# Kernel optimization log

Hardware: AMD Instinct MI355X
Metric: run time of the kernel (lower is better)

## Reference

```python
import jax, jax.numpy as jnp
import numpy as np

B, N, D = 4, 512, 128
H1, H2 = 64, 32
NEG_SLOPE = 0.1

def _leaky(x):
    return jnp.where(x >= 0, x, NEG_SLOPE * x)

def setup_inputs() -> dict:
    key = jax.random.key(0)
    ks = jax.random.split(key, 7)
    v = jax.random.normal(ks[0], (B, N, D), dtype=jnp.float32)
    # 1x1 Conv2d weights collapse to [out, in] matrices
    W1 = jax.random.normal(ks[1], (H1, D), dtype=jnp.float32) * (1.0 / np.sqrt(D))
    b1 = jax.random.normal(ks[2], (H1,), dtype=jnp.float32) * 0.01
    W2 = jax.random.normal(ks[3], (H2, H1), dtype=jnp.float32) * (1.0 / np.sqrt(H1))
    b2 = jax.random.normal(ks[4], (H2,), dtype=jnp.float32) * 0.01
    W3 = jax.random.normal(ks[5], (1, H2), dtype=jnp.float32) * (1.0 / np.sqrt(H2))
    b3 = jax.random.normal(ks[6], (1,), dtype=jnp.float32) * 0.01
    return {"v": v, "W1": W1, "b1": b1, "W2": W2, "b2": b2, "W3": W3, "b3": b3}

def reference(v, W1, b1, W2, b2, W3, b3):
    # phi_ij = |v_i - v_j|  -> (B, N, N, D)
    phi = jnp.abs(v[:, :, None, :] - v[:, None, :, :])
    # 1x1 convs == per-(i,j) linear layers over the channel dim
    h = _leaky(jnp.einsum('bijd,od->bijo', phi, W1) + b1)   # (B,N,N,64)
    h = _leaky(jnp.einsum('bijc,oc->bijo', h, W2) + b2)     # (B,N,N,32)
    a = jnp.einsum('bijc,oc->bijo', h, W3) + b3             # (B,N,N,1)
    a = a[..., 0]                                           # (B,N,N)
    return jax.nn.softmax(a, axis=2)                        # softmax over neighbors j
```

## Files before the change

### kernel.cpp

```cpp
#include <hip/hip_runtime.h>

#define NN  512
#define DD  128
#define NTASK_B 8448
#define NWAVES  2048

typedef __attribute__((ext_vector_type(4))) float f32x4;
typedef __attribute__((ext_vector_type(8))) short s16x8;

#define MFMA(a, b, c) __builtin_amdgcn_mfma_f32_16x16x32_bf16((a), (b), (c), 0, 0, 0)

#define B1S 136
#define B2S 72
#define H1S 68

__device__ inline void split8(const float* __restrict__ x, s16x8& h, s16x8& l) {
    uint4 hp, lp;
    unsigned* hw = (unsigned*)&hp;
    unsigned* lw = (unsigned*)&lp;
    #pragma unroll
    for (int i = 0; i < 4; ++i) {
        float x0 = x[2 * i], x1 = x[2 * i + 1];
        unsigned t0 = __float_as_uint(x0) + 0x8000u;
        unsigned t1 = __float_as_uint(x1) + 0x8000u;
        hw[i] = __builtin_amdgcn_perm(t1, t0, 0x07060302u);
        float l0 = x0 - __uint_as_float(t0 & 0xFFFF0000u);
        float l1 = x1 - __uint_as_float(t1 & 0xFFFF0000u);
        lw[i] = __builtin_amdgcn_perm(__float_as_uint(l1), __float_as_uint(l0), 0x07060302u);
    }
    h = __builtin_bit_cast(s16x8, hp);
    l = __builtin_bit_cast(s16x8, lp);
}

__device__ inline void split1(float x, unsigned short& hs, unsigned short& ls) {
    unsigned t = __float_as_uint(x) + 0x8000u;
    hs = (unsigned short)(t >> 16);
    float lo = x - __uint_as_float(t & 0xFFFF0000u);
    ls = (unsigned short)(__float_as_uint(lo) >> 16);
}

__global__ __launch_bounds__(256, 2)
void adj_sym(const float* __restrict__ v,
             const float* __restrict__ W1,
             const float* __restrict__ b1,
             const float* __restrict__ W2,
             const float* __restrict__ b2,
             const float* __restrict__ W3,
             const float* __restrict__ b3,
             float* __restrict__ out)
{
    __shared__ __attribute__((aligned(16))) unsigned short B1h_s[64 * B1S];
    __shared__ __attribute__((aligned(16))) unsigned short B1l_s[64 * B1S];
    __shared__ __attribute__((aligned(16))) unsigned short B2h_s[32 * B2S];
    __shared__ __attribute__((aligned(16))) unsigned short B2l_s[32 * B2S];
    __shared__ __attribute__((aligned(16))) float h1_s[64 * H1S];

    const int t    = threadIdx.x;
    const int w    = t >> 6;
    const int lane = t & 63;
    const int m16  = t & 15;
    const int q    = (t & 63) >> 4;
    const int q8   = q * 8;

    #pragma unroll
    for (int e = 0; e < 32; ++e) {
        int idx = e * 256 + t;
        unsigned short hs, ls;
        split1(W1[idx], hs, ls);
        int o = idx >> 7, d = idx & 127;
        B1h_s[o * B1S + d] = hs;
        B1l_s[o * B1S + d] = ls;
    }
    #pragma unroll
    for (int e = 0; e < 8; ++e) {
        int idx = e * 256 + t;
        unsigned short hs, ls;
        split1(W2[idx], hs, ls);
        int c2 = idx >> 6, k = idx & 63;
        B2h_s[c2 * B2S + k] = hs;
        B2l_s[c2 * B2S + k] = ls;
    }

    float b1v[4];
    #pragma unroll
    for (int ot = 0; ot < 4; ++ot) b1v[ot] = b1[ot * 16 + m16];
    const float b2v0 = b2[m16];
    const float b2v1 = b2[16 + m16];
    const float w3v0 = W3[m16];
    const float w3v1 = W3[16 + m16];
    const float b3v  = b3[0];

    __syncthreads();

    const int g    = blockIdx.x * 4 + w;
    int       tk   = (33 * g) >> 1;
    const int tend = (33 * (g + 1)) >> 1;

    unsigned bb = (unsigned)tk / (unsigned)NTASK_B;
    int r = tk - (int)(bb * NTASK_B);
    int G = (int)((__fsqrt_rn((float)(2 * r + 1)) - 1.0f) * 0.25f);
    if (G < 0) G = 0;
    while (8 * (G + 1) * (G + 2) <= r) ++G;
    while (G > 0 && 8 * G * (G + 1) > r) --G;
    int rem = r - 8 * G * (G + 1);
    int s   = rem / (G + 1);
    int gj  = rem - s * (G + 1);
    bool newi = true;

    float yv[4][8];

    #pragma unroll 1
    for (; tk < tend; ++tk) {
        const int    i  = (G << 4) + s;
        const int    j0 = gj << 4;
        const size_t vb = ((size_t)bb << 9);

        if (newi) {
            const float* __restrict__ vip = v + (vb + i) * DD;
            #pragma unroll
            for (int kt = 0; kt < 4; ++kt) {
                *(float4*)&yv[kt][0] = *(const float4*)(vip + kt * 32 + q8);
                *(float4*)&yv[kt][4] = *(const float4*)(vip + kt * 32 + q8 + 4);
            }
        }

        const float* __restrict__ vr = v + (vb + j0 + m16) * DD;
        float xr[4][8];
        #pragma unroll
        for (int kt = 0; kt < 4; ++kt) {
            *(float4*)&xr[kt][0] = *(const float4*)(vr + kt * 32 + q8);
            *(float4*)&xr[kt][4] = *(const float4*)(vr + kt * 32 + q8 + 4);
        }

        f32x4 c[4];
        #pragma unroll
        for (int ot = 0; ot < 4; ++ot) c[ot] = (f32x4){0.f, 0.f, 0.f, 0.f};

        #pragma unroll
        for (int kt = 0; kt < 4; ++kt) {
            float d8[8];
            #pragma unroll
            for (int ii = 0; ii < 8; ++ii) d8[ii] = fabsf(yv[kt][ii] - xr[kt][ii]);
            s16x8 ah, al;
            split8(d8, ah, al);
            #pragma unroll
            for (int ot = 0; ot < 4; ++ot) {
                const int n = ot * 16 + m16;
                s16x8 bh = *(const s16x8*)(B1h_s + n * B1S + kt * 32 + q8);
                s16x8 bl = *(const s16x8*)(B1l_s + n * B1S + kt * 32 + q8);
                c[ot] = MFMA(ah, bh, c[ot]);
                c[ot] = MFMA(al, bh, c[ot]);
                c[ot] = MFMA(ah, bl, c[ot]);
            }
        }

        #pragma unroll
        for (int ot = 0; ot < 4; ++ot)
            #pragma unroll
            for (int rr = 0; rr < 4; ++rr) {
                float hv = c[ot][rr] + b1v[ot];
                hv = fmaxf(hv, 0.1f * hv);
                h1_s[(w * 16 + q * 4 + rr) * H1S + ot * 16 + m16] = hv;
            }

        f32x4 dacc[2];
        dacc[0] = (f32x4){0.f, 0.f, 0.f, 0.f};
        dacc[1] = (f32x4){0.f, 0.f, 0.f, 0.f};
        #pragma unroll
        for (int kt2 = 0; kt2 < 2; ++kt2) {
            const float* hp = h1_s + (w * 16 + m16) * H1S + kt2 * 32 + q8;
            float a8[8];
            *(float4*)&a8[0] = *(const float4*)(hp);
            *(float4*)&a8[4] = *(const float4*)(hp + 4);
            s16x8 ah, al;
            split8(a8, ah, al);
            #pragma unroll
            for (int ot2 = 0; ot2 < 2; ++ot2) {
                const int n = ot2 * 16 + m16;
                s16x8 bh = *(const s16x8*)(B2h_s + n * B2S + kt2 * 32 + q8);
                s16x8 bl = *(const s16x8*)(B2l_s + n * B2S + kt2 * 32 + q8);
                dacc[ot2] = MFMA(ah, bh, dacc[ot2]);
                dacc[ot2] = MFMA(al, bh, dacc[ot2]);
                dacc[ot2] = MFMA(ah, bl, dacc[ot2]);
            }
        }

        float sval[4];
        #pragma unroll
        for (int r2 = 0; r2 < 4; ++r2) {
            float h0  = dacc[0][r2] + b2v0;  h0  = fmaxf(h0, 0.1f * h0);
            float h1v = dacc[1][r2] + b2v1;  h1v = fmaxf(h1v, 0.1f * h1v);
            float sc = fmaf(w3v0, h0, w3v1 * h1v);
            sc += __shfl_xor(sc, 1, 64);
            sc += __shfl_xor(sc, 2, 64);
            sc += __shfl_xor(sc, 4, 64);
            sc += __shfl_xor(sc, 8, 64);
            sval[r2] = sc + b3v;
        }
        const int p = lane & 15;
        float vv = sval[0];
        vv = ((lane & 3) == 1) ? sval[1] : vv;
        vv = ((lane & 3) == 2) ? sval[2] : vv;
        vv = ((lane & 3) == 3) ? sval[3] : vv;
        const float pv = __shfl(vv, ((p >> 2) << 4) | (p & 3), 64);

        if (lane < 32) {
            const size_t addr = (lane < 16)
                ? (vb + (unsigned)i) * NN + (unsigned)(j0 + p)
                : (vb + (unsigned)(j0 + p)) * NN + (unsigned)i;
            out[addr] = pv;
        }

        ++gj;
        newi = false;
        if (gj > G) {
            gj = 0; newi = true;
            if (++s == 16) {
                s = 0;
                if (++G == 32) { G = 0; ++bb; }
            }
        }
    }
}

__global__ __launch_bounds__(256)
void row_softmax(float* __restrict__ out)
{
    __shared__ float red[8];
    const int t    = threadIdx.x;
    const int w    = t >> 6;
    const int lane = t & 63;

    float* orow = out + (size_t)blockIdx.x * NN;
    float a0 = orow[t];
    float a1 = orow[t + 256];

    float m = fmaxf(a0, a1);
    #pragma unroll
    for (int sh = 32; sh > 0; sh >>= 1)
        m = fmaxf(m, __shfl_xor(m, sh, 64));
    if (lane == 0) red[w] = m;
    __syncthreads();
    const float M = fmaxf(fmaxf(red[0], red[1]), fmaxf(red[2], red[3]));

    float e0 = __expf(a0 - M);
    float e1 = __expf(a1 - M);
    float s01 = e0 + e1;
    #pragma unroll
    for (int sh = 32; sh > 0; sh >>= 1)
        s01 += __shfl_xor(s01, sh, 64);
    if (lane == 0) red[4 + w] = s01;
    __syncthreads();
    const float S = (red[4] + red[5]) + (red[6] + red[7]);
    const float inv = 1.0f / S;

    orow[t]       = e0 * inv;
    orow[t + 256] = e1 * inv;
}

extern "C" void kernel_launch(void* const* d_in, const int* in_sizes, int n_in,
                              void* d_out, int out_size, void* d_ws, size_t ws_size,
                              hipStream_t stream) {
    const float* v  = (const float*)d_in[0];
    const float* W1 = (const float*)d_in[1];
    const float* b1 = (const float*)d_in[2];
    const float* W2 = (const float*)d_in[3];
    const float* b2 = (const float*)d_in[4];
    const float* W3 = (const float*)d_in[5];
    const float* b3 = (const float*)d_in[6];
    float* out = (float*)d_out;

    adj_sym<<<dim3(512), dim3(256), 0, stream>>>(v, W1, b1, W2, b2, W3, b3, out);
    row_softmax<<<dim3(4 * NN), dim3(256), 0, stream>>>(out);
}
```

Measured before the change: 118.0 us.

## Process two j-tiles per task and keep W2 split fragments in registers

Each wave task now covers 32 neighbour columns (two 16-wide j tiles) instead of 16. The two tiles share the B1 shared-memory fragment loads, and their MFMAs are interleaved to hide latency. W2 hi/lo bf16 fragments move from LDS into registers, h1 is stored in LDS pre-packed as hi/lo pairs, and the cross-lane reductions use DPP row rotates instead of shuffles. The task count and decode change to match. The costs are higher register pressure and wasted MFMA work on the odd diagonal tile, whose second half is computed but not stored.

```diff
diff --git a/kernel.cpp b/kernel.cpp
--- a/kernel.cpp
+++ b/kernel.cpp
@@ -2,8 +2,7 @@
 
 #define NN  512
 #define DD  128
-#define NTASK_B 8448
-#define NWAVES  2048
+#define NST_B 4352
 
 typedef __attribute__((ext_vector_type(4))) float f32x4;
 typedef __attribute__((ext_vector_type(8))) short s16x8;
@@ -11,8 +10,10 @@
 #define MFMA(a, b, c) __builtin_amdgcn_mfma_f32_16x16x32_bf16((a), (b), (c), 0, 0, 0)
 
 #define B1S 136
-#define B2S 72
 #define H1S 68
+
+#define ROR_ADD(x, CTRL) \
+    ((x) + __int_as_float(__builtin_amdgcn_update_dpp(0, __float_as_int(x), (CTRL), 0xF, 0xF, true)))
 
 __device__ inline void split8(const float* __restrict__ x, s16x8& h, s16x8& l) {
     uint4 hp, lp;
@@ -32,28 +33,38 @@
     l = __builtin_bit_cast(s16x8, lp);
 }
 
-__device__ inline void split1(float x, unsigned short& hs, unsigned short& ls) {
-    unsigned t = __float_as_uint(x) + 0x8000u;
-    hs = (unsigned short)(t >> 16);
-    float lo = x - __uint_as_float(t & 0xFFFF0000u);
-    ls = (unsigned short)(__float_as_uint(lo) >> 16);
+__device__ inline unsigned packhl(float x) {
+    unsigned tt = __float_as_uint(x) + 0x8000u;
+    float lo = x - __uint_as_float(tt & 0xFFFF0000u);
+    return __builtin_amdgcn_perm(__float_as_uint(lo), tt, 0x07060302u);
+}
+
+__device__ inline void unpack8(const unsigned* __restrict__ u, s16x8& h, s16x8& l) {
+    uint4 hp, lp;
+    unsigned* hw = (unsigned*)&hp;
+    unsigned* lw = (unsigned*)&lp;
+    #pragma unroll
+    for (int i = 0; i < 4; ++i) {
+        hw[i] = __builtin_amdgcn_perm(u[2 * i + 1], u[2 * i], 0x05040100u);
+        lw[i] = __builtin_amdgcn_perm(u[2 * i + 1], u[2 * i], 0x07060302u);
+    }
+    h = __builtin_bit_cast(s16x8, hp);
+    l = __builtin_bit_cast(s16x8, lp);
 }
 
 __global__ __launch_bounds__(256, 2)
-void adj_sym(const float* __restrict__ v,
-             const float* __restrict__ W1,
-             const float* __restrict__ b1,
-             const float* __restrict__ W2,
-             const float* __restrict__ b2,
-             const float* __restrict__ W3,
-             const float* __restrict__ b3,
-             float* __restrict__ out)
+void adj_sym2(const float* __restrict__ v,
+              const float* __restrict__ W1,
+              const float* __restrict__ b1,
+              const float* __restrict__ W2,
+              const float* __restrict__ b2,
+              const float* __restrict__ W3,
+              const float* __restrict__ b3,
+              float* __restrict__ out)
 {
     __shared__ __attribute__((aligned(16))) unsigned short B1h_s[64 * B1S];
     __shared__ __attribute__((aligned(16))) unsigned short B1l_s[64 * B1S];
-    __shared__ __attribute__((aligned(16))) unsigned short B2h_s[32 * B2S];
-    __shared__ __attribute__((aligned(16))) unsigned short B2l_s[32 * B2S];
-    __shared__ __attribute__((aligned(16))) float h1_s[64 * H1S];
+    __shared__ __attribute__((aligned(16))) unsigned h1p_s[64 * H1S];
 
     const int t    = threadIdx.x;
     const int w    = t >> 6;
@@ -63,23 +74,39 @@
     const int q8   = q * 8;
 
     #pragma unroll
-    for (int e = 0; e < 32; ++e) {
-        int idx = e * 256 + t;
-        unsigned short hs, ls;
-        split1(W1[idx], hs, ls);
-        int o = idx >> 7, d = idx & 127;
-        B1h_s[o * B1S + d] = hs;
-        B1l_s[o * B1S + d] = ls;
+    for (int e = 0; e < 8; ++e) {
+        int idx4 = e * 256 + t;
+        int o = idx4 >> 5;
+        int d = (idx4 & 31) * 4;
+        float4 x = *(const float4*)(W1 + idx4 * 4);
+        float xs[4] = {x.x, x.y, x.z, x.w};
+        unsigned tb[4], lb[4];
+        #pragma unroll
+        for (int k2 = 0; k2 < 4; ++k2) {
+            tb[k2] = __float_as_uint(xs[k2]) + 0x8000u;
+            float lo = xs[k2] - __uint_as_float(tb[k2] & 0xFFFF0000u);
+            lb[k2] = __float_as_uint(lo);
+        }
+        uint2 hw, lw;
+        hw.x = __builtin_amdgcn_perm(tb[1], tb[0], 0x07060302u);
+        hw.y = __builtin_amdgcn_perm(tb[3], tb[2], 0x07060302u);
+        lw.x = __builtin_amdgcn_perm(lb[1], lb[0], 0x07060302u);
+        lw.y = __builtin_amdgcn_perm(lb[3], lb[2], 0x07060302u);
+        *(uint2*)(B1h_s + o * B1S + d) = hw;
+        *(uint2*)(B1l_s + o * B1S + d) = lw;
     }
-    #pragma unroll
-    for (int e = 0; e < 8; ++e) {
-        int idx = e * 256 + t;
-        unsigned short hs, ls;
-        split1(W2[idx], hs, ls);
-        int c2 = idx >> 6, k = idx & 63;
-        B2h_s[c2 * B2S + k] = hs;
-        B2l_s[c2 * B2S + k] = ls;
-    }
+
+    s16x8 B2h_r[2][2], B2l_r[2][2];
+    #pragma unroll
+    for (int kt2 = 0; kt2 < 2; ++kt2)
+        #pragma unroll
+        for (int ot2 = 0; ot2 < 2; ++ot2) {
+            const float* wp = W2 + (ot2 * 16 + m16) * 64 + kt2 * 32 + q8;
+            float a8[8];
+            *(float4*)&a8[0] = *(const float4*)wp;
+            *(float4*)&a8[4] = *(const float4*)(wp + 4);
+            split8(a8, B2h_r[kt2][ot2], B2l_r[kt2][ot2]);
+        }
 
     float b1v[4];
     #pragma unroll
@@ -93,30 +120,33 @@
     __syncthreads();
 
     const int g    = blockIdx.x * 4 + w;
-    int       tk   = (33 * g) >> 1;
-    const int tend = (33 * (g + 1)) >> 1;
-
-    unsigned bb = (unsigned)tk / (unsigned)NTASK_B;
-    int r = tk - (int)(bb * NTASK_B);
-    int G = (int)((__fsqrt_rn((float)(2 * r + 1)) - 1.0f) * 0.25f);
+    int       tk   = (17 * g) >> 1;
+    const int tend = (17 * (g + 1)) >> 1;
+
+    unsigned bb = (unsigned)tk / (unsigned)NST_B;
+    int r = tk - (int)(bb * NST_B);
+    int G = (int)__fsqrt_rn((float)r * 0.25f + 1.0f) - 1;
     if (G < 0) G = 0;
-    while (8 * (G + 1) * (G + 2) <= r) ++G;
-    while (G > 0 && 8 * G * (G + 1) > r) --G;
-    int rem = r - 8 * G * (G + 1);
-    int s   = rem / (G + 1);
-    int gj  = rem - s * (G + 1);
+    if (G > 31) G = 31;
+    while (G < 31 && 16 * (((G + 2) * (G + 2)) >> 2) <= r) ++G;
+    while (G > 0 && 16 * (((G + 1) * (G + 1)) >> 2) > r) --G;
+    int rem = r - 16 * (((G + 1) * (G + 1)) >> 2);
+    int nG  = (G >> 1) + 1;
+    int s   = rem / nG;
+    int gj2 = rem - s * nG;
     bool newi = true;
 
     float yv[4][8];
 
     #pragma unroll 1
     for (; tk < tend; ++tk) {
+        const size_t vb = (size_t)bb << 9;
         const int    i  = (G << 4) + s;
-        const int    j0 = gj << 4;
-        const size_t vb = ((size_t)bb << 9);
+        const int    j0 = gj2 << 5;
+        const bool   v2 = (2 * gj2 + 1) <= G;
 
         if (newi) {
-            const float* __restrict__ vip = v + (vb + i) * DD;
+            const float* __restrict__ vip = v + (vb + (unsigned)i) * DD;
             #pragma unroll
             for (int kt = 0; kt < 4; ++kt) {
                 *(float4*)&yv[kt][0] = *(const float4*)(vip + kt * 32 + q8);
@@ -124,100 +154,113 @@
             }
         }
 
-        const float* __restrict__ vr = v + (vb + j0 + m16) * DD;
-        float xr[4][8];
+        const float* __restrict__ vrA = v + (vb + (unsigned)(j0 + m16)) * DD;
+        const float* __restrict__ vrB = vrA + 16 * DD;
+        float xrA[4][8], xrB[4][8];
         #pragma unroll
         for (int kt = 0; kt < 4; ++kt) {
-            *(float4*)&xr[kt][0] = *(const float4*)(vr + kt * 32 + q8);
-            *(float4*)&xr[kt][4] = *(const float4*)(vr + kt * 32 + q8 + 4);
-        }
-
-        f32x4 c[4];
-        #pragma unroll
-        for (int ot = 0; ot < 4; ++ot) c[ot] = (f32x4){0.f, 0.f, 0.f, 0.f};
+            *(float4*)&xrA[kt][0] = *(const float4*)(vrA + kt * 32 + q8);
+            *(float4*)&xrA[kt][4] = *(const float4*)(vrA + kt * 32 + q8 + 4);
+            *(float4*)&xrB[kt][0] = *(const float4*)(vrB + kt * 32 + q8);
+            *(float4*)&xrB[kt][4] = *(const float4*)(vrB + kt * 32 + q8 + 4);
+        }
+
+        f32x4 cA[4], cB[4];
+        #pragma unroll
+        for (int ot = 0; ot < 4; ++ot) {
+            cA[ot] = (f32x4){0.f, 0.f, 0.f, 0.f};
+            cB[ot] = (f32x4){0.f, 0.f, 0.f, 0.f};
+        }
 
         #pragma unroll
         for (int kt = 0; kt < 4; ++kt) {
             float d8[8];
-            #pragma unroll
-            for (int ii = 0; ii < 8; ++ii) d8[ii] = fabsf(yv[kt][ii] - xr[kt][ii]);
-            s16x8 ah, al;
-            split8(d8, ah, al);
+            s16x8 ahA, alA, ahB, alB;
+            #pragma unroll
+            for (int ii = 0; ii < 8; ++ii) d8[ii] = fabsf(yv[kt][ii] - xrA[kt][ii]);
+            split8(d8, ahA, alA);
+            #pragma unroll
+            for (int ii = 0; ii < 8; ++ii) d8[ii] = fabsf(yv[kt][ii] - xrB[kt][ii]);
+            split8(d8, ahB, alB);
             #pragma unroll
             for (int ot = 0; ot < 4; ++ot) {
                 const int n = ot * 16 + m16;
                 s16x8 bh = *(const s16x8*)(B1h_s + n * B1S + kt * 32 + q8);
                 s16x8 bl = *(const s16x8*)(B1l_s + n * B1S + kt * 32 + q8);
-                c[ot] = MFMA(ah, bh, c[ot]);
-                c[ot] = MFMA(al, bh, c[ot]);
-                c[ot] = MFMA(ah, bl, c[ot]);
-            }
-        }
-
-        #pragma unroll
-        for (int ot = 0; ot < 4; ++ot)
-            #pragma unroll
-            for (int rr = 0; rr < 4; ++rr) {
-                float hv = c[ot][rr] + b1v[ot];
-                hv = fmaxf(hv, 0.1f * hv);
-                h1_s[(w * 16 + q * 4 + rr) * H1S + ot * 16 + m16] = hv;
-            }
-
-        f32x4 dacc[2];
-        dacc[0] = (f32x4){0.f, 0.f, 0.f, 0.f};
-        dacc[1] = (f32x4){0.f, 0.f, 0.f, 0.f};
-        #pragma unroll
-        for (int kt2 = 0; kt2 < 2; ++kt2) {
-            const float* hp = h1_s + (w * 16 + m16) * H1S + kt2 * 32 + q8;
-            float a8[8];
-            *(float4*)&a8[0] = *(const float4*)(hp);
-            *(float4*)&a8[4] = *(const float4*)(hp + 4);
-            s16x8 ah, al;
-            split8(a8, ah, al);
-            #pragma unroll
-            for (int ot2 = 0; ot2 < 2; ++ot2) {
-                const int n = ot2 * 16 + m16;
-                s16x8 bh = *(const s16x8*)(B2h_s + n * B2S + kt2 * 32 + q8);
-                s16x8 bl = *(const s16x8*)(B2l_s + n * B2S + kt2 * 32 + q8);
-                dacc[ot2] = MFMA(ah, bh, dacc[ot2]);
-                dacc[ot2] = MFMA(al, bh, dacc[ot2]);
-                dacc[ot2] = MFMA(ah, bl, dacc[ot2]);
-            }
-        }
-
-        float sval[4];
-        #pragma unroll
-        for (int r2 = 0; r2 < 4; ++r2) {
-            float h0  = dacc[0][r2] + b2v0;  h0  = fmaxf(h0, 0.1f * h0);
-            float h1v = dacc[1][r2] + b2v1;  h1v = fmaxf(h1v, 0.1f * h1v);
-            float sc = fmaf(w3v0, h0, w3v1 * h1v);
-            sc += __shfl_xor(sc, 1, 64);
-            sc += __shfl_xor(sc, 2, 64);
-            sc += __shfl_xor(sc, 4, 64);
-            sc += __shfl_xor(sc, 8, 64);
-            sval[r2] = sc + b3v;
-        }
-        const int p = lane & 15;
-        float vv = sval[0];
-        vv = ((lane & 3) == 1) ? sval[1] : vv;
-        vv = ((lane & 3) == 2) ? sval[2] : vv;
-        vv = ((lane & 3) == 3) ? sval[3] : vv;
-        const float pv = __shfl(vv, ((p >> 2) << 4) | (p & 3), 64);
-
-        if (lane < 32) {
-            const size_t addr = (lane < 16)
-                ? (vb + (unsigned)i) * NN + (unsigned)(j0 + p)
-                : (vb + (unsigned)(j0 + p)) * NN + (unsigned)i;
-            out[addr] = pv;
-        }
-
-        ++gj;
-        newi = false;
-        if (gj > G) {
-            gj = 0; newi = true;
+                cA[ot] = MFMA(ahA, bh, cA[ot]);
+                cB[ot] = MFMA(ahB, bh, cB[ot]);
+                cA[ot] = MFMA(alA, bh, cA[ot]);
+                cB[ot] = MFMA(alB, bh, cB[ot]);
+                cA[ot] = MFMA(ahA, bl, cA[ot]);
+                cB[ot] = MFMA(ahB, bl, cB[ot]);
+            }
+        }
+
+        auto tail = [&](f32x4 (&c)[4], int jt, bool doStore) {
+            #pragma unroll
+            for (int ot = 0; ot < 4; ++ot)
+                #pragma unroll
+                for (int rr = 0; rr < 4; ++rr) {
+                    float hv = c[ot][rr] + b1v[ot];
+                    hv = fmaxf(hv, 0.1f * hv);
+                    h1p_s[(w * 16 + q * 4 + rr) * H1S + ot * 16 + m16] = packhl(hv);
+                }
+
+            f32x4 dacc0 = (f32x4){0.f, 0.f, 0.f, 0.f};
+            f32x4 dacc1 = (f32x4){0.f, 0.f, 0.f, 0.f};
+            #pragma unroll
+            for (int kt2 = 0; kt2 < 2; ++kt2) {
+                const unsigned* hp = h1p_s + (w * 16 + m16) * H1S + kt2 * 32 + q8;
+                unsigned u[8];
+                *(uint4*)&u[0] = *(const uint4*)hp;
+                *(uint4*)&u[4] = *(const uint4*)(hp + 4);
+                s16x8 ah, al;
+                unpack8(u, ah, al);
+                dacc0 = MFMA(ah, B2h_r[kt2][0], dacc0);
+                dacc1 = MFMA(ah, B2h_r[kt2][1], dacc1);
+                dacc0 = MFMA(al, B2h_r[kt2][0], dacc0);
+                dacc1 = MFMA(al, B2h_r[kt2][1], dacc1);
+                dacc0 = MFMA(ah, B2l_r[kt2][0], dacc0);
+                dacc1 = MFMA(ah, B2l_r[kt2][1], dacc1);
+            }
+
+            float sval[4];
+            #pragma unroll
+            for (int r2 = 0; r2 < 4; ++r2) {
+                float h0  = dacc0[r2] + b2v0;  h0  = fmaxf(h0, 0.1f * h0);
+                float h1v = dacc1[r2] + b2v1;  h1v = fmaxf(h1v, 0.1f * h1v);
+                float sc = fmaf(w3v0, h0, w3v1 * h1v);
+                sc = ROR_ADD(sc, 0x121);
+                sc = ROR_ADD(sc, 0x122);
+                sc = ROR_ADD(sc, 0x124);
+                sc = ROR_ADD(sc, 0x128);
+                sval[r2] = sc + b3v;
+            }
+            const int p = lane & 15;
+            float vv = sval[0];
+            vv = ((lane & 3) == 1) ? sval[1] : vv;
+            vv = ((lane & 3) == 2) ? sval[2] : vv;
+            vv = ((lane & 3) == 3) ? sval[3] : vv;
+            const float pv = __shfl(vv, ((p >> 2) << 4) | (p & 3), 64);
+
+            if (doStore && lane < 32) {
+                const size_t addr = (lane < 16)
+                    ? (vb + (unsigned)i) * NN + (unsigned)(jt + p)
+                    : (vb + (unsigned)(jt + p)) * NN + (unsigned)i;
+                out[addr] = pv;
+            }
+        };
+
+        tail(cA, j0, true);
+        if (v2) tail(cB, j0 + 16, true);
+
+        ++gj2; newi = false;
+        if (gj2 == nG) {
+            gj2 = 0; newi = true;
             if (++s == 16) {
                 s = 0;
                 if (++G == 32) { G = 0; ++bb; }
+                nG = (G >> 1) + 1;
             }
         }
     }
@@ -270,6 +313,6 @@
     const float* b3 = (const float*)d_in[6];
     float* out = (float*)d_out;
 
-    adj_sym<<<dim3(512), dim3(256), 0, stream>>>(v, W1, b1, W2, b2, W3, b3, out);
+    adj_sym2<<<dim3(512), dim3(256), 0, stream>>>(v, W1, b1, W2, b2, W3, b3, out);
     row_softmax<<<dim3(4 * NN), dim3(256), 0, stream>>>(out);
 }
```

Result: slower. 148.6 us (+25.9%).

## Use 6-wave blocks, pre-split h1 in LDS, DPP row reductions

Applied to the files above, without the earlier changes.

Blocks grow from 4 to 6 waves, each wave taking a fixed 11 tasks (3072 waves in total), with launch bounds changed to 384 threads and 3 blocks per CU. The first-layer activations are split into bf16 hi/lo once when written to LDS, as a packed word, so the second layer only needs perm unpacks instead of a full re-split. The 16-lane score reduction uses DPP row_ror adds instead of shfl_xor, and W1 is staged with float4 loads. The aim is better occupancy and fewer ALU and LDS-permute operations, at the cost of tighter register limits and a larger shared-memory footprint.

```diff
diff --git a/kernel.cpp b/kernel.cpp
--- a/kernel.cpp
+++ b/kernel.cpp
@@ -3,7 +3,6 @@
 #define NN  512
 #define DD  128
 #define NTASK_B 8448
-#define NWAVES  2048
 
 typedef __attribute__((ext_vector_type(4))) float f32x4;
 typedef __attribute__((ext_vector_type(8))) short s16x8;
@@ -14,7 +13,10 @@
 #define B2S 72
 #define H1S 68
 
-__device__ inline void split8(const float* __restrict__ x, s16x8& h, s16x8& l) {
+#define ROR_ADD(x, CTRL) \
+    ((x) + __int_as_float(__builtin_amdgcn_update_dpp(0, __float_as_int(x), (CTRL), 0xF, 0xF, true)))
+
+__device__ __forceinline__ void split8(const float* __restrict__ x, s16x8& h, s16x8& l) {
     uint4 hp, lp;
     unsigned* hw = (unsigned*)&hp;
     unsigned* lw = (unsigned*)&lp;
@@ -32,28 +34,47 @@
     l = __builtin_bit_cast(s16x8, lp);
 }
 
-__device__ inline void split1(float x, unsigned short& hs, unsigned short& ls) {
-    unsigned t = __float_as_uint(x) + 0x8000u;
-    hs = (unsigned short)(t >> 16);
-    float lo = x - __uint_as_float(t & 0xFFFF0000u);
+__device__ __forceinline__ void split1(float x, unsigned short& hs, unsigned short& ls) {
+    unsigned tt = __float_as_uint(x) + 0x8000u;
+    hs = (unsigned short)(tt >> 16);
+    float lo = x - __uint_as_float(tt & 0xFFFF0000u);
     ls = (unsigned short)(__float_as_uint(lo) >> 16);
 }
 
-__global__ __launch_bounds__(256, 2)
-void adj_sym(const float* __restrict__ v,
-             const float* __restrict__ W1,
-             const float* __restrict__ b1,
-             const float* __restrict__ W2,
-             const float* __restrict__ b2,
-             const float* __restrict__ W3,
-             const float* __restrict__ b3,
-             float* __restrict__ out)
+__device__ __forceinline__ unsigned packhl(float x) {
+    unsigned tt = __float_as_uint(x) + 0x8000u;
+    float lo = x - __uint_as_float(tt & 0xFFFF0000u);
+    return __builtin_amdgcn_perm(__float_as_uint(lo), tt, 0x07060302u);
+}
+
+__device__ __forceinline__ void unpack8(const unsigned* __restrict__ u, s16x8& h, s16x8& l) {
+    uint4 hp, lp;
+    unsigned* hw = (unsigned*)&hp;
+    unsigned* lw = (unsigned*)&lp;
+    #pragma unroll
+    for (int i = 0; i < 4; ++i) {
+        hw[i] = __builtin_amdgcn_perm(u[2 * i + 1], u[2 * i], 0x05040100u);
+        lw[i] = __builtin_amdgcn_perm(u[2 * i + 1], u[2 * i], 0x07060302u);
+    }
+    h = __builtin_bit_cast(s16x8, hp);
+    l = __builtin_bit_cast(s16x8, lp);
+}
+
+__global__ __launch_bounds__(384, 3)
+void adj_sym7(const float* __restrict__ v,
+              const float* __restrict__ W1,
+              const float* __restrict__ b1,
+              const float* __restrict__ W2,
+              const float* __restrict__ b2,
+              const float* __restrict__ W3,
+              const float* __restrict__ b3,
+              float* __restrict__ out)
 {
     __shared__ __attribute__((aligned(16))) unsigned short B1h_s[64 * B1S];
     __shared__ __attribute__((aligned(16))) unsigned short B1l_s[64 * B1S];
     __shared__ __attribute__((aligned(16))) unsigned short B2h_s[32 * B2S];
     __shared__ __attribute__((aligned(16))) unsigned short B2l_s[32 * B2S];
-    __shared__ __attribute__((aligned(16))) float h1_s[64 * H1S];
+    __shared__ __attribute__((aligned(16))) unsigned h1p_s[96 * H1S];
 
     const int t    = threadIdx.x;
     const int w    = t >> 6;
@@ -63,22 +84,40 @@
     const int q8   = q * 8;
 
     #pragma unroll
-    for (int e = 0; e < 32; ++e) {
-        int idx = e * 256 + t;
-        unsigned short hs, ls;
-        split1(W1[idx], hs, ls);
-        int o = idx >> 7, d = idx & 127;
-        B1h_s[o * B1S + d] = hs;
-        B1l_s[o * B1S + d] = ls;
-    }
-    #pragma unroll
-    for (int e = 0; e < 8; ++e) {
-        int idx = e * 256 + t;
-        unsigned short hs, ls;
-        split1(W2[idx], hs, ls);
-        int c2 = idx >> 6, k = idx & 63;
-        B2h_s[c2 * B2S + k] = hs;
-        B2l_s[c2 * B2S + k] = ls;
+    for (int e = 0; e < 6; ++e) {
+        int idx4 = e * 384 + t;
+        if (idx4 < 2048) {
+            int o = idx4 >> 5;
+            int d = (idx4 & 31) * 4;
+            float4 x = *(const float4*)(W1 + idx4 * 4);
+            float xs[4] = {x.x, x.y, x.z, x.w};
+            unsigned tb[4], lb[4];
+            #pragma unroll
+            for (int k2 = 0; k2 < 4; ++k2) {
+                tb[k2] = __float_as_uint(xs[k2]) + 0x8000u;
+                float lo = xs[k2] - __uint_as_float(tb[k2] & 0xFFFF0000u);
+                lb[k2] = __float_as_uint(lo);
+            }
+            uint2 hw, lw;
+            hw.x = __builtin_amdgcn_perm(tb[1], tb[0], 0x07060302u);
+            hw.y = __builtin_amdgcn_perm(tb[3], tb[2], 0x07060302u);
+            lw.x = __builtin_amdgcn_perm(lb[1], lb[0], 0x07060302u);
+            lw.y = __builtin_amdgcn_perm(lb[3], lb[2], 0x07060302u);
+            *(uint2*)(B1h_s + o * B1S + d) = hw;
+            *(uint2*)(B1l_s + o * B1S + d) = lw;
+        }
+    }
+
+    #pragma unroll
+    for (int e = 0; e < 6; ++e) {
+        int idx = e * 384 + t;
+        if (idx < 2048) {
+            unsigned short hs, ls;
+            split1(W2[idx], hs, ls);
+            int c2 = idx >> 6, k = idx & 63;
+            B2h_s[c2 * B2S + k] = hs;
+            B2l_s[c2 * B2S + k] = ls;
+        }
     }
 
     float b1v[4];
@@ -92,9 +131,9 @@
 
     __syncthreads();
 
-    const int g    = blockIdx.x * 4 + w;
-    int       tk   = (33 * g) >> 1;
-    const int tend = (33 * (g + 1)) >> 1;
+    const int g    = blockIdx.x * 6 + w;
+    int       tk   = 11 * g;
+    const int tend = tk + 11;
 
     unsigned bb = (unsigned)tk / (unsigned)NTASK_B;
     int r = tk - (int)(bb * NTASK_B);
@@ -111,12 +150,12 @@
 
     #pragma unroll 1
     for (; tk < tend; ++tk) {
+        const size_t vb = (size_t)bb << 9;
         const int    i  = (G << 4) + s;
         const int    j0 = gj << 4;
-        const size_t vb = ((size_t)bb << 9);
 
         if (newi) {
-            const float* __restrict__ vip = v + (vb + i) * DD;
+            const float* __restrict__ vip = v + (vb + (unsigned)i) * DD;
             #pragma unroll
             for (int kt = 0; kt < 4; ++kt) {
                 *(float4*)&yv[kt][0] = *(const float4*)(vip + kt * 32 + q8);
@@ -124,7 +163,7 @@
             }
         }
 
-        const float* __restrict__ vr = v + (vb + j0 + m16) * DD;
+        const float* __restrict__ vr = v + (vb + (unsigned)(j0 + m16)) * DD;
         float xr[4][8];
         #pragma unroll
         for (int kt = 0; kt < 4; ++kt) {
@@ -160,48 +199,68 @@
             for (int rr = 0; rr < 4; ++rr) {
                 float hv = c[ot][rr] + b1v[ot];
                 hv = fmaxf(hv, 0.1f * hv);
-                h1_s[(w * 16 + q * 4 + rr) * H1S + ot * 16 + m16] = hv;
-            }
-
-        f32x4 dacc[2];
-        dacc[0] = (f32x4){0.f, 0.f, 0.f, 0.f};
-        dacc[1] = (f32x4){0.f, 0.f, 0.f, 0.f};
+                h1p_s[(w * 16 + q * 4 + rr) * H1S + ot * 16 + m16] = packhl(hv);
+            }
+
+        f32x4 dacc0 = (f32x4){0.f, 0.f, 0.f, 0.f};
+        f32x4 dacc1 = (f32x4){0.f, 0.f, 0.f, 0.f};
         #pragma unroll
         for (int kt2 = 0; kt2 < 2; ++kt2) {
-            const float* hp = h1_s + (w * 16 + m16) * H1S + kt2 * 32 + q8;
-            float a8[8];
-            *(float4*)&a8[0] = *(const float4*)(hp);
-            *(float4*)&a8[4] = *(const float4*)(hp + 4);
+            const unsigned* hp = h1p_s + (w * 16 + m16) * H1S + kt2 * 32 + q8;
+            unsigned u[8];
+            *(uint4*)&u[0] = *(const uint4*)hp;
+            *(uint4*)&u[4] = *(const uint4*)(hp + 4);
             s16x8 ah, al;
-            split8(a8, ah, al);
-            #pragma unroll
-            for (int ot2 = 0; ot2 < 2; ++ot2) {
-                const int n = ot2 * 16 + m16;
-                s16x8 bh = *(const s16x8*)(B2h_s + n * B2S + kt2 * 32 + q8);
-                s16x8 bl = *(const s16x8*)(B2l_s + n * B2S + kt2 * 32 + q8);
-                dacc[ot2] = MFMA(ah, bh, dacc[ot2]);
-                dacc[ot2] = MFMA(al, bh, dacc[ot2]);
-                dacc[ot2] = MFMA(ah, bl, dacc[ot2]);
-            }
-        }
-
-        float sval[4];
-        #pragma unroll
-        for (int r2 = 0; r2 < 4; ++r2) {
-            float h0  = dacc[0][r2] + b2v0;  h0  = fmaxf(h0, 0.1f * h0);
-            float h1v = dacc[1][r2] + b2v1;  h1v = fmaxf(h1v, 0.1f * h1v);
-            float sc = fmaf(w3v0, h0, w3v1 * h1v);
-            sc += __shfl_xor(sc, 1, 64);
-            sc += __shfl_xor(sc, 2, 64);
-            sc += __shfl_xor(sc, 4, 64);
-            sc += __shfl_xor(sc, 8, 64);
-            sval[r2] = sc + b3v;
+            unpack8(u, ah, al);
+            {
+                s16x8 bh = *(const s16x8*)(B2h_s + m16 * B2S + kt2 * 32 + q8);
+                s16x8 bl = *(const s16x8*)(B2l_s + m16 * B2S + kt2 * 32 + q8);
+                dacc0 = MFMA(ah, bh, dacc0);
+                dacc0 = MFMA(al, bh, dacc0);
+                dacc0 = MFMA(ah, bl, dacc0);
+            }
+            {
+                s16x8 bh = *(const s16x8*)(B2h_s + (16 + m16) * B2S + kt2 * 32 + q8);
+                s16x8 bl = *(const s16x8*)(B2l_s + (16 + m16) * B2S + kt2 * 32 + q8);
+                dacc1 = MFMA(ah, bh, dacc1);
+                dacc1 = MFMA(al, bh, dacc1);
+                dacc1 = MFMA(ah, bl, dacc1);
+            }
+        }
+
+        float sval0, sval1, sval2, sval3;
+        {
+            float h0, h1v, sc;
+            h0 = dacc0[0] + b2v0;  h0 = fmaxf(h0, 0.1f * h0);
+            h1v = dacc1[0] + b2v1; h1v = fmaxf(h1v, 0.1f * h1v);
+            sc = fmaf(w3v0, h0, w3v1 * h1v);
+            sc = ROR_ADD(sc, 0x121); sc = ROR_ADD(sc, 0x122);
+            sc = ROR_ADD(sc, 0x124); sc = ROR_ADD(sc, 0x128);
+            sval0 = sc + b3v;
+            h0 = dacc0[1] + b2v0;  h0 = fmaxf(h0, 0.1f * h0);
+            h1v = dacc1[1] + b2v1; h1v = fmaxf(h1v, 0.1f * h1v);
+            sc = fmaf(w3v0, h0, w3v1 * h1v);
+            sc = ROR_ADD(sc, 0x121); sc = ROR_ADD(sc, 0x122);
+            sc = ROR_ADD(sc, 0x124); sc = ROR_ADD(sc, 0x128);
+            sval1 = sc + b3v;
+            h0 = dacc0[2] + b2v0;  h0 = fmaxf(h0, 0.1f * h0);
+            h1v = dacc1[2] + b2v1; h1v = fmaxf(h1v, 0.1f * h1v);
+            sc = fmaf(w3v0, h0, w3v1 * h1v);
+            sc = ROR_ADD(sc, 0x121); sc = ROR_ADD(sc, 0x122);
+            sc = ROR_ADD(sc, 0x124); sc = ROR_ADD(sc, 0x128);
+            sval2 = sc + b3v;
+            h0 = dacc0[3] + b2v0;  h0 = fmaxf(h0, 0.1f * h0);
+            h1v = dacc1[3] + b2v1; h1v = fmaxf(h1v, 0.1f * h1v);
+            sc = fmaf(w3v0, h0, w3v1 * h1v);
+            sc = ROR_ADD(sc, 0x121); sc = ROR_ADD(sc, 0x122);
+            sc = ROR_ADD(sc, 0x124); sc = ROR_ADD(sc, 0x128);
+            sval3 = sc + b3v;
         }
         const int p = lane & 15;
-        float vv = sval[0];
-        vv = ((lane & 3) == 1) ? sval[1] : vv;
-        vv = ((lane & 3) == 2) ? sval[2] : vv;
-        vv = ((lane & 3) == 3) ? sval[3] : vv;
+        float vv = sval0;
+        vv = ((lane & 3) == 1) ? sval1 : vv;
+        vv = ((lane & 3) == 2) ? sval2 : vv;
+        vv = ((lane & 3) == 3) ? sval3 : vv;
         const float pv = __shfl(vv, ((p >> 2) << 4) | (p & 3), 64);
 
         if (lane < 32) {
@@ -270,6 +329,6 @@
     const float* b3 = (const float*)d_in[6];
     float* out = (float*)d_out;
 
-    adj_sym<<<dim3(512), dim3(256), 0, stream>>>(v, W1, b1, W2, b2, W3, b3, out);
+    adj_sym7<<<dim3(512), dim3(384), 0, stream>>>(v, W1, b1, W2, b2, W3, b3, out);
     row_softmax<<<dim3(4 * NN), dim3(256), 0, stream>>>(out);
 }
```

Result: slower. 292.7 us (+148.1%).
